# Performance work log

Measured on AMD Instinct MI355X. Metric: run time of the kernel, lower is better.

The kernel has to match this reference:

```python
import jax, jax.numpy as jnp
import numpy as np

NEG_SLOPE = 0.2  # PyG GATConv default leaky_relu slope


def gat_conv(x, src, dst, W, a_src, a_dst, b, num_nodes):
    """One PyG-style GATConv layer (concat over heads).
    x: [N, F_in]; src/dst: [E] (message flows src -> dst);
    W: [F_in, H*C]; a_src/a_dst: [H, C]; b: [H*C].
    """
    H, C = a_src.shape
    h = (x @ W).reshape(num_nodes, H, C)              # [N, H, C]
    alpha_src = jnp.sum(h * a_src, axis=-1)           # [N, H]
    alpha_dst = jnp.sum(h * a_dst, axis=-1)           # [N, H]
    e = jax.nn.leaky_relu(alpha_src[src] + alpha_dst[dst], NEG_SLOPE)  # [E, H]
    # segment softmax over incoming edges of each destination node
    m = jax.ops.segment_max(e, dst, num_segments=num_nodes)            # [N, H]
    ex = jnp.exp(e - m[dst])
    s = jax.ops.segment_sum(ex, dst, num_segments=num_nodes)           # [N, H]
    alpha = ex / (s[dst] + 1e-16)                                      # [E, H]
    msg = h[src] * alpha[:, :, None]                                   # [E, H, C]
    out = jax.ops.segment_sum(msg, dst, num_segments=num_nodes)        # [N, H, C]
    return out.reshape(num_nodes, H * C) + b


def setup_inputs() -> dict:
    key = jax.random.key(0)
    ks = jax.random.split(key, 12)
    N, E, F_in, C, H = 50000, 800000, 256, 64, 8
    x = jax.random.normal(ks[0], (N, F_in), dtype=jnp.float32)
    edge_index = jax.random.randint(ks[1], (2, E), 0, N, dtype=jnp.int64)
    glorot = lambda k, shape: jax.random.normal(k, shape, jnp.float32) * np.sqrt(2.0 / (shape[0] + shape[-1]))
    return {
        "x": x,
        "edge_index": edge_index,
        "W1": glorot(ks[2], (F_in, H * C)),
        "att_src1": glorot(ks[3], (H, C)),
        "att_dst1": glorot(ks[4], (H, C)),
        "b1": jnp.zeros((H * C,), jnp.float32),
        "W2": glorot(ks[5], (H * C, 1 * C)),
        "att_src2": glorot(ks[6], (1, C)),
        "att_dst2": glorot(ks[7], (1, C)),
        "b2": jnp.zeros((C,), jnp.float32),
    }


def reference(x, edge_index, W1, att_src1, att_dst1, b1, W2, att_src2, att_dst2, b2):
    N = x.shape[0]
    # add self-loops (PyG GATConv default add_self_loops=True)
    loops = jnp.arange(N, dtype=edge_index.dtype)
    src = jnp.concatenate([edge_index[0], loops])
    dst = jnp.concatenate([edge_index[1], loops])
    h = gat_conv(x, src, dst, W1, att_src1, att_dst1, b1, N)   # [N, 512]
    h = jax.nn.relu(h)                                         # dropout p=0 -> identity
    out = gat_conv(h, src, dst, W2, att_src2, att_dst2, b2, N) # [N, 64]
    return out
```

## Files before the change

kernel.cpp:

```cpp
#include <hip/hip_runtime.h>
#include <hip/hip_bf16.h>
#include <math.h>
#include <type_traits>

#define NEG_SLOPE 0.2f
#define CAP 64

typedef float f32x4 __attribute__((ext_vector_type(4)));
typedef short s16x8 __attribute__((ext_vector_type(8)));
typedef short s16x4 __attribute__((ext_vector_type(4)));

__device__ __forceinline__ float bf2f(ushort s) {
    union { unsigned u; float f; } cv; cv.u = ((unsigned)s) << 16;
    return cv.f;
}
__device__ __forceinline__ ushort f2bf(float f) {
    __hip_bfloat16 b = __float2bfloat16(f);
    union { __hip_bfloat16 b; ushort u; } cv; cv.b = b;
    return cv.u;
}

__device__ __forceinline__ int edge_val(const int* e, long long i, int is64) {
    return is64 ? e[(size_t)(2 * i)] : e[(size_t)i];
}

__global__ __launch_bounds__(256) void prep_k(
        const float* __restrict__ x, ushort* __restrict__ xb, int NX,
        const float* __restrict__ W1, ushort* __restrict__ W1t, int K1, int N1,
        const float* __restrict__ W2, ushort* __restrict__ W2t, int K2, int N2,
        int nbX, int nbW1) {
    int b = blockIdx.x, tid = threadIdx.x;
    if (b < nbX) {
        int base = (b * 256 + tid) * 8;
        if (base + 8 <= NX) {
            float4 v0 = *(const float4*)&x[base];
            float4 v1 = *(const float4*)&x[base + 4];
            s16x8 w;
            w[0] = (short)f2bf(v0.x); w[1] = (short)f2bf(v0.y);
            w[2] = (short)f2bf(v0.z); w[3] = (short)f2bf(v0.w);
            w[4] = (short)f2bf(v1.x); w[5] = (short)f2bf(v1.y);
            w[6] = (short)f2bf(v1.z); w[7] = (short)f2bf(v1.w);
            *(s16x8*)&xb[base] = w;
        }
        return;
    }
    b -= nbX;
    if (b < nbW1) {
        int idx = b * 256 + tid;
        if (idx < K1 * N1) {
            int k = idx & (K1 - 1), n = idx / K1;
            W1t[(size_t)n * K1 + k] = f2bf(W1[(size_t)k * N1 + n]);
        }
        return;
    }
    b -= nbW1;
    {
        int idx = b * 256 + tid;
        if (idx < K2 * N2) {
            int k = idx & (K2 - 1), n = idx / K2;
            W2t[(size_t)n * K2 + k] = f2bf(W2[(size_t)k * N2 + n]);
        }
    }
}

__global__ __launch_bounds__(256) void scatter_k(
        const int* __restrict__ ebuf, int E, int Nn,
        int* __restrict__ counts, int* __restrict__ csr) {
    __shared__ int s_is64;
    if (threadIdx.x < 64) {
        int v = ebuf[2 * threadIdx.x + 1];
        unsigned long long bl = __ballot(v != 0);
        if (threadIdx.x == 0) s_is64 = (bl == 0ull) ? 1 : 0;
    }
    __syncthreads();
    int is64 = s_is64;
    int i = blockIdx.x * 256 + threadIdx.x;
    if (i >= E + Nn) return;
    int s, d;
    if (i < E) {
        s = edge_val(ebuf, i, is64);
        d = edge_val(ebuf, (long long)E + i, is64);
    } else {
        s = i - E; d = s;
    }
    int pos = atomicAdd(&counts[d], 1);
    if (pos < CAP) csr[(size_t)d * CAP + pos] = s;
}

template <int KK, int NCOLS, int H, int HB>
__global__ __launch_bounds__(512) void gemm_bres(
        const ushort* __restrict__ A, const ushort* __restrict__ Bt,
        ushort* __restrict__ C,
        const float* __restrict__ att_s, const float* __restrict__ att_d,
        float* __restrict__ as_, float* __restrict__ ad_,
        int M, int Ntot) {
    constexpr int NT = NCOLS / 16;
    __shared__ __align__(16) ushort Bs[NCOLS][KK + 8];

    int tid = threadIdx.x;
    int wid = tid >> 6, lane = tid & 63;
    int l15 = lane & 15, l4 = lane >> 4;
    int bx = blockIdx.x, by = blockIdx.y;
    int bn = bx * NCOLS;

#pragma unroll
    for (int p = 0; p < NCOLS * KK / (8 * 512); ++p) {
        int idx = p * 512 + tid;
        int n = idx / (KK / 8);
        int kc = (idx % (KK / 8)) << 3;
        *(s16x8*)&Bs[n][kc] = *(const s16x8*)&Bt[(size_t)(bn + n) * KK + kc];
    }

    int mbase = by * 128 + wid * 16;
    int rowA = mbase + l15; if (rowA >= M) rowA = M - 1;
    const ushort* Ap = A + (size_t)rowA * KK + (l4 << 3);
    s16x8 af[KK / 32];
#pragma unroll
    for (int ks = 0; ks < KK / 32; ++ks) af[ks] = *(const s16x8*)&Ap[ks * 32];

    __syncthreads();

    f32x4 acc[NT] = {};
#pragma unroll
    for (int nt = 0; nt < NT; ++nt) {
#pragma unroll
        for (int ks = 0; ks < KK / 32; ++ks) {
            s16x8 bfr = *(const s16x8*)&Bs[nt * 16 + l15][ks * 32 + (l4 << 3)];
            acc[nt] = __builtin_amdgcn_mfma_f32_16x16x32_bf16(af[ks], bfr, acc[nt], 0, 0, 0);
        }
    }

#pragma unroll
    for (int h = 0; h < HB; ++h) {
        int head = bx * HB + h;
        float asv[4], adv[4];
#pragma unroll
        for (int t = 0; t < 4; ++t) {
            asv[t] = att_s[head * 64 + t * 16 + l15];
            adv[t] = att_d[head * 64 + t * 16 + l15];
        }
#pragma unroll
        for (int j = 0; j < 4; ++j) {
            int r = mbase + (l4 << 2) + j;
            float ps = 0.f, pd = 0.f;
#pragma unroll
            for (int t = 0; t < 4; ++t) {
                float v = acc[h * 4 + t][j];
                ps += v * asv[t];
                pd += v * adv[t];
            }
#pragma unroll
            for (int off = 1; off < 16; off <<= 1) {
                ps += __shfl_xor(ps, off);
                pd += __shfl_xor(pd, off);
            }
            if (r < M) {
                if (l15 == 0) {
                    as_[(size_t)r * H + head] = ps;
                    ad_[(size_t)r * H + head] = pd;
                }
#pragma unroll
                for (int t = 0; t < 4; ++t)
                    C[(size_t)r * Ntot + head * 64 + t * 16 + l15] = f2bf(acc[h * 4 + t][j]);
            }
        }
    }
}

__global__ __launch_bounds__(256) void gat_fused_l1(
        const ushort* __restrict__ h, const float* __restrict__ as_,
        const float* __restrict__ ad_, const int* __restrict__ counts,
        const int* __restrict__ csr, const float* __restrict__ bias,
        ushort* __restrict__ out1, int N) {
    int n = (blockIdx.x * 256 + threadIdx.x) >> 6;
    if (n >= N) return;
    int l = threadIdx.x & 63;
    size_t base = (size_t)n * CAP;
    int deg = counts[n]; deg = deg > CAP ? CAP : deg;

    int hh = l & 7, e0 = l >> 3;
    float adw = ad_[n * 8 + hh];
    float m = -1e30f, s = 0.f;
    for (int k = e0; k < deg; k += 8) {
        int src = csr[base + k];
        float e = as_[src * 8 + hh] + adw;
        e = e > 0.f ? e : NEG_SLOPE * e;
        float mn = fmaxf(m, e);
        s = s * __expf(m - mn) + __expf(e - mn);
        m = mn;
    }
#pragma unroll
    for (int off = 8; off < 64; off <<= 1) {
        float mo = __shfl_xor(m, off), so = __shfl_xor(s, off);
        float mn = fmaxf(m, mo);
        s = s * __expf(m - mn) + so * __expf(mo - mn);
        m = mn;
    }
    float inv = 1.f / (s + 1e-16f);
    int hd = l >> 3;
    float mh   = __shfl(m, hd);
    float invh = __shfl(inv, hd);
    float adh  = __shfl(adw, hd);

    float acc[8] = {};
    int k = 0;
    for (; k + 4 <= deg; k += 4) {
        int s0 = csr[base + k],     s1 = csr[base + k + 1];
        int s2 = csr[base + k + 2], s3 = csr[base + k + 3];
        s16x8 v0 = *(const s16x8*)&h[((size_t)s0 << 9) + (l << 3)];
        s16x8 v1 = *(const s16x8*)&h[((size_t)s1 << 9) + (l << 3)];
        s16x8 v2 = *(const s16x8*)&h[((size_t)s2 << 9) + (l << 3)];
        s16x8 v3 = *(const s16x8*)&h[((size_t)s3 << 9) + (l << 3)];
        float e0v = as_[s0 * 8 + hd] + adh;
        float e1v = as_[s1 * 8 + hd] + adh;
        float e2v = as_[s2 * 8 + hd] + adh;
        float e3v = as_[s3 * 8 + hd] + adh;
        e0v = e0v > 0.f ? e0v : NEG_SLOPE * e0v;
        e1v = e1v > 0.f ? e1v : NEG_SLOPE * e1v;
        e2v = e2v > 0.f ? e2v : NEG_SLOPE * e2v;
        e3v = e3v > 0.f ? e3v : NEG_SLOPE * e3v;
        float a0 = __expf(e0v - mh);
        float a1 = __expf(e1v - mh);
        float a2 = __expf(e2v - mh);
        float a3 = __expf(e3v - mh);
#pragma unroll
        for (int j = 0; j < 8; ++j)
            acc[j] += a0 * bf2f((ushort)v0[j]) + a1 * bf2f((ushort)v1[j])
                    + a2 * bf2f((ushort)v2[j]) + a3 * bf2f((ushort)v3[j]);
    }
    for (; k < deg; ++k) {
        int s0 = csr[base + k];
        s16x8 v0 = *(const s16x8*)&h[((size_t)s0 << 9) + (l << 3)];
        float e0v = as_[s0 * 8 + hd] + adh;
        e0v = e0v > 0.f ? e0v : NEG_SLOPE * e0v;
        float a0 = __expf(e0v - mh);
#pragma unroll
        for (int j = 0; j < 8; ++j) acc[j] += a0 * bf2f((ushort)v0[j]);
    }
    float4 b0 = *(const float4*)&bias[l * 8];
    float4 b1 = *(const float4*)&bias[l * 8 + 4];
    s16x8 w;
    w[0] = f2bf(fmaxf(acc[0] * invh + b0.x, 0.f));
    w[1] = f2bf(fmaxf(acc[1] * invh + b0.y, 0.f));
    w[2] = f2bf(fmaxf(acc[2] * invh + b0.z, 0.f));
    w[3] = f2bf(fmaxf(acc[3] * invh + b0.w, 0.f));
    w[4] = f2bf(fmaxf(acc[4] * invh + b1.x, 0.f));
    w[5] = f2bf(fmaxf(acc[5] * invh + b1.y, 0.f));
    w[6] = f2bf(fmaxf(acc[6] * invh + b1.z, 0.f));
    w[7] = f2bf(fmaxf(acc[7] * invh + b1.w, 0.f));
    *(s16x8*)&out1[((size_t)n << 9) + (l << 3)] = w;
}

__global__ __launch_bounds__(256) void gat_fused_l2(
        const ushort* __restrict__ h, const float* __restrict__ as_,
        const float* __restrict__ ad_, const int* __restrict__ counts,
        const int* __restrict__ csr, const float* __restrict__ bias,
        float* __restrict__ out, int N) {
    int n = (blockIdx.x * 256 + threadIdx.x) >> 6;
    if (n >= N) return;
    int l = threadIdx.x & 63;
    size_t base = (size_t)n * CAP;
    int deg = counts[n]; deg = deg > CAP ? CAP : deg;
    float adv = ad_[n];

    float m = -1e30f, s = 0.f;
    for (int k = l; k < deg; k += 64) {
        float e = as_[csr[base + k]] + adv;
        e = e > 0.f ? e : NEG_SLOPE * e;
        float mn = fmaxf(m, e);
        s = s * __expf(m - mn) + __expf(e - mn);
        m = mn;
    }
#pragma unroll
    for (int off = 1; off < 64; off <<= 1) {
        float mo = __shfl_xor(m, off), so = __shfl_xor(s, off);
        float mn = fmaxf(m, mo);
        s = s * __expf(m - mn) + so * __expf(mo - mn);
        m = mn;
    }
    float inv = 1.f / (s + 1e-16f);

    int q = l >> 4, c4 = l & 15;
    float a0 = 0.f, a1 = 0.f, a2 = 0.f, a3 = 0.f;
    int k = q;
    for (; k + 12 < deg; k += 16) {
        int sA = csr[base + k],     sB = csr[base + k + 4];
        int sC = csr[base + k + 8], sD = csr[base + k + 12];
        s16x4 vA = *(const s16x4*)&h[((size_t)sA << 6) + (c4 << 2)];
        s16x4 vB = *(const s16x4*)&h[((size_t)sB << 6) + (c4 << 2)];
        s16x4 vC = *(const s16x4*)&h[((size_t)sC << 6) + (c4 << 2)];
        s16x4 vD = *(const s16x4*)&h[((size_t)sD << 6) + (c4 << 2)];
        float eA = as_[sA] + adv, eB = as_[sB] + adv;
        float eC = as_[sC] + adv, eD = as_[sD] + adv;
        eA = eA > 0.f ? eA : NEG_SLOPE * eA;
        eB = eB > 0.f ? eB : NEG_SLOPE * eB;
        eC = eC > 0.f ? eC : NEG_SLOPE * eC;
        eD = eD > 0.f ? eD : NEG_SLOPE * eD;
        float aA = __expf(eA - m), aB = __expf(eB - m);
        float aC = __expf(eC - m), aD = __expf(eD - m);
        a0 += aA * bf2f((ushort)vA[0]) + aB * bf2f((ushort)vB[0])
            + aC * bf2f((ushort)vC[0]) + aD * bf2f((ushort)vD[0]);
        a1 += aA * bf2f((ushort)vA[1]) + aB * bf2f((ushort)vB[1])
            + aC * bf2f((ushort)vC[1]) + aD * bf2f((ushort)vD[1]);
        a2 += aA * bf2f((ushort)vA[2]) + aB * bf2f((ushort)vB[2])
            + aC * bf2f((ushort)vC[2]) + aD * bf2f((ushort)vD[2]);
        a3 += aA * bf2f((ushort)vA[3]) + aB * bf2f((ushort)vB[3])
            + aC * bf2f((ushort)vC[3]) + aD * bf2f((ushort)vD[3]);
    }
    for (; k < deg; k += 4) {
        int sA = csr[base + k];
        s16x4 vA = *(const s16x4*)&h[((size_t)sA << 6) + (c4 << 2)];
        float eA = as_[sA] + adv;
        eA = eA > 0.f ? eA : NEG_SLOPE * eA;
        float aA = __expf(eA - m);
        a0 += aA * bf2f((ushort)vA[0]);
        a1 += aA * bf2f((ushort)vA[1]);
        a2 += aA * bf2f((ushort)vA[2]);
        a3 += aA * bf2f((ushort)vA[3]);
    }
    a0 += __shfl_xor(a0, 16); a0 += __shfl_xor(a0, 32);
    a1 += __shfl_xor(a1, 16); a1 += __shfl_xor(a1, 32);
    a2 += __shfl_xor(a2, 16); a2 += __shfl_xor(a2, 32);
    a3 += __shfl_xor(a3, 16); a3 += __shfl_xor(a3, 32);
    if (q == 0) {
        float4 bv = *(const float4*)&bias[c4 << 2];
        float4 r;
        r.x = a0 * inv + bv.x; r.y = a1 * inv + bv.y;
        r.z = a2 * inv + bv.z; r.w = a3 * inv + bv.w;
        *(float4*)&out[((size_t)n << 6) + (c4 << 2)] = r;
    }
}

extern "C" void kernel_launch(void* const* d_in, const int* in_sizes, int n_in,
                              void* d_out, int out_size, void* d_ws, size_t ws_size,
                              hipStream_t stream) {
    const float* x    = (const float*)d_in[0];
    const int*   ebuf = (const int*)d_in[1];
    const float* W1   = (const float*)d_in[2];
    const float* aS1  = (const float*)d_in[3];
    const float* aD1  = (const float*)d_in[4];
    const float* b1   = (const float*)d_in[5];
    const float* W2   = (const float*)d_in[6];
    const float* aS2  = (const float*)d_in[7];
    const float* aD2  = (const float*)d_in[8];
    const float* b2   = (const float*)d_in[9];
    float* out = (float*)d_out;

    const int F_in = 256, H1 = 8, HC1 = 512, C2 = 64;
    int N = in_sizes[0] / F_in;
    int E = in_sizes[1] / 2;
    int NX = N * F_in;

    char* ws = (char*)d_ws;
    size_t off = 0;
    auto alloc = [&](size_t bytes) -> void* {
        void* p = ws + off;
        off = (off + bytes + 255) & ~(size_t)255;
        return p;
    };
    ushort* h1b    = (ushort*)alloc((size_t)N * HC1 * 2);
    ushort* out1b  = (ushort*)alloc((size_t)N * HC1 * 2);
    float* as1     = (float*)alloc((size_t)N * H1 * 4);
    float* ad1     = (float*)alloc((size_t)N * H1 * 4);
    float* as2     = (float*)alloc((size_t)N * 4);
    float* ad2     = (float*)alloc((size_t)N * 4);
    int*   counts  = (int*)alloc((size_t)N * 4);
    int*   csr     = (int*)alloc((size_t)N * CAP * 4);
    ushort* W1t    = (ushort*)alloc((size_t)F_in * HC1 * 2);
    ushort* W2t    = (ushort*)alloc((size_t)HC1 * C2 * 2);
    ushort* h2b    = h1b;
    ushort* xb     = out1b;

    int nbX  = (NX + 2047) / 2048;
    int nbW1 = (F_in * HC1 + 255) >> 8;
    int nbW2 = (HC1 * C2 + 255) >> 8;
    int nbScat = (E + N + 255) / 256;

    hipMemsetAsync(counts, 0, (size_t)N * 4, stream);

    prep_k<<<nbX + nbW1 + nbW2, 256, 0, stream>>>(
        x, xb, NX, W1, W1t, F_in, HC1, W2, W2t, HC1, C2, nbX, nbW1);

    scatter_k<<<nbScat, 256, 0, stream>>>(ebuf, E, N, counts, csr);

    {
        dim3 g(2, (N + 127) / 128);
        gemm_bres<256, 256, 8, 4><<<g, 512, 0, stream>>>(
            xb, W1t, h1b, aS1, aD1, as1, ad1, N, HC1);
    }

    gat_fused_l1<<<(N + 3) / 4, 256, 0, stream>>>(h1b, as1, ad1, counts, csr, b1, out1b, N);

    {
        dim3 g(1, (N + 127) / 128);
        gemm_bres<512, 64, 1, 1><<<g, 512, 0, stream>>>(
            out1b, W2t, h2b, aS2, aD2, as2, ad2, N, C2);
    }

    gat_fused_l2<<<(N + 3) / 4, 256, 0, stream>>>(h2b, as2, ad2, counts, csr, b2, out, N);
}
```

Baseline: 306.6 us.

## Fuse x bf16 conversion into GEMM1 and co-launch edge scatter with it

The separate x-to-bf16 conversion pass is removed: GEMM1 now reads fp32 x directly and converts it in registers. The CSR scatter kernel is merged into the same launch as GEMM1, so scatter blocks can run alongside GEMM blocks, and the counts memset moves into the weight-prep kernel. GEMM block indices are remapped so the two column tiles sharing a row block are scheduled near each other for A reuse. In exchange, GEMM1 reads twice as many bytes of A, and a shared-memory allocation may now be reserved for scatter blocks too.

After: 288.0 us. -6.1%, faster.

```diff
diff --git a/kernel.cpp b/kernel.cpp
--- a/kernel.cpp
+++ b/kernel.cpp
@@ -25,26 +25,10 @@
 }
 
 __global__ __launch_bounds__(256) void prep_k(
-        const float* __restrict__ x, ushort* __restrict__ xb, int NX,
         const float* __restrict__ W1, ushort* __restrict__ W1t, int K1, int N1,
         const float* __restrict__ W2, ushort* __restrict__ W2t, int K2, int N2,
-        int nbX, int nbW1) {
+        int* __restrict__ counts, int N, int nbW1, int nbW2) {
     int b = blockIdx.x, tid = threadIdx.x;
-    if (b < nbX) {
-        int base = (b * 256 + tid) * 8;
-        if (base + 8 <= NX) {
-            float4 v0 = *(const float4*)&x[base];
-            float4 v1 = *(const float4*)&x[base + 4];
-            s16x8 w;
-            w[0] = (short)f2bf(v0.x); w[1] = (short)f2bf(v0.y);
-            w[2] = (short)f2bf(v0.z); w[3] = (short)f2bf(v0.w);
-            w[4] = (short)f2bf(v1.x); w[5] = (short)f2bf(v1.y);
-            w[6] = (short)f2bf(v1.z); w[7] = (short)f2bf(v1.w);
-            *(s16x8*)&xb[base] = w;
-        }
-        return;
-    }
-    b -= nbX;
     if (b < nbW1) {
         int idx = b * 256 + tid;
         if (idx < K1 * N1) {
@@ -54,53 +38,31 @@
         return;
     }
     b -= nbW1;
-    {
+    if (b < nbW2) {
         int idx = b * 256 + tid;
         if (idx < K2 * N2) {
             int k = idx & (K2 - 1), n = idx / K2;
             W2t[(size_t)n * K2 + k] = f2bf(W2[(size_t)k * N2 + n]);
         }
-    }
-}
-
-__global__ __launch_bounds__(256) void scatter_k(
-        const int* __restrict__ ebuf, int E, int Nn,
-        int* __restrict__ counts, int* __restrict__ csr) {
-    __shared__ int s_is64;
-    if (threadIdx.x < 64) {
-        int v = ebuf[2 * threadIdx.x + 1];
-        unsigned long long bl = __ballot(v != 0);
-        if (threadIdx.x == 0) s_is64 = (bl == 0ull) ? 1 : 0;
-    }
-    __syncthreads();
-    int is64 = s_is64;
-    int i = blockIdx.x * 256 + threadIdx.x;
-    if (i >= E + Nn) return;
-    int s, d;
-    if (i < E) {
-        s = edge_val(ebuf, i, is64);
-        d = edge_val(ebuf, (long long)E + i, is64);
-    } else {
-        s = i - E; d = s;
-    }
-    int pos = atomicAdd(&counts[d], 1);
-    if (pos < CAP) csr[(size_t)d * CAP + pos] = s;
-}
-
-template <int KK, int NCOLS, int H, int HB>
-__global__ __launch_bounds__(512) void gemm_bres(
-        const ushort* __restrict__ A, const ushort* __restrict__ Bt,
+        return;
+    }
+    b -= nbW2;
+    int i = b * 256 + tid;
+    if (i < N) counts[i] = 0;
+}
+
+template <typename AT, int KK, int NCOLS, int H, int HB>
+__device__ __forceinline__ void gemm_bres_core(
+        int bx, int by, const AT* __restrict__ A, const ushort* __restrict__ Bt,
         ushort* __restrict__ C,
         const float* __restrict__ att_s, const float* __restrict__ att_d,
-        float* __restrict__ as_, float* __restrict__ ad_,
-        int M, int Ntot) {
+        float* __restrict__ as_, float* __restrict__ ad_, int M, int Ntot) {
     constexpr int NT = NCOLS / 16;
     __shared__ __align__(16) ushort Bs[NCOLS][KK + 8];
 
     int tid = threadIdx.x;
     int wid = tid >> 6, lane = tid & 63;
     int l15 = lane & 15, l4 = lane >> 4;
-    int bx = blockIdx.x, by = blockIdx.y;
     int bn = bx * NCOLS;
 
 #pragma unroll
@@ -113,10 +75,25 @@
 
     int mbase = by * 128 + wid * 16;
     int rowA = mbase + l15; if (rowA >= M) rowA = M - 1;
-    const ushort* Ap = A + (size_t)rowA * KK + (l4 << 3);
     s16x8 af[KK / 32];
-#pragma unroll
-    for (int ks = 0; ks < KK / 32; ++ks) af[ks] = *(const s16x8*)&Ap[ks * 32];
+    if constexpr (std::is_same_v<AT, float>) {
+        const float* Ap = A + (size_t)rowA * KK + (l4 << 3);
+#pragma unroll
+        for (int ks = 0; ks < KK / 32; ++ks) {
+            float4 u0 = *(const float4*)&Ap[ks * 32];
+            float4 u1 = *(const float4*)&Ap[ks * 32 + 4];
+            s16x8 w;
+            w[0] = (short)f2bf(u0.x); w[1] = (short)f2bf(u0.y);
+            w[2] = (short)f2bf(u0.z); w[3] = (short)f2bf(u0.w);
+            w[4] = (short)f2bf(u1.x); w[5] = (short)f2bf(u1.y);
+            w[6] = (short)f2bf(u1.z); w[7] = (short)f2bf(u1.w);
+            af[ks] = w;
+        }
+    } else {
+        const ushort* Ap = A + (size_t)rowA * KK + (l4 << 3);
+#pragma unroll
+        for (int ks = 0; ks < KK / 32; ++ks) af[ks] = *(const s16x8*)&Ap[ks * 32];
+    }
 
     __syncthreads();
 
@@ -165,6 +142,52 @@
             }
         }
     }
+}
+
+__global__ __launch_bounds__(512) void gemm1_scatter(
+        const float* __restrict__ A, const ushort* __restrict__ Bt,
+        ushort* __restrict__ C, const float* __restrict__ att_s,
+        const float* __restrict__ att_d, float* __restrict__ as_,
+        float* __restrict__ ad_, int M, int Ntot, int nby, int nGemm,
+        const int* __restrict__ ebuf, int E, int Nn,
+        int* __restrict__ counts, int* __restrict__ csr) {
+    int g = blockIdx.x;
+    if (g < nGemm) {
+        int by = (g & 7) + ((g >> 4) << 3);
+        int bx = (g >> 3) & 1;
+        if (by < nby)
+            gemm_bres_core<float, 256, 256, 8, 4>(bx, by, A, Bt, C,
+                                                  att_s, att_d, as_, ad_, M, Ntot);
+        return;
+    }
+    __shared__ int s_is64;
+    if (threadIdx.x < 64) {
+        int v = ebuf[2 * threadIdx.x + 1];
+        unsigned long long bl = __ballot(v != 0);
+        if (threadIdx.x == 0) s_is64 = (bl == 0ull) ? 1 : 0;
+    }
+    __syncthreads();
+    int is64 = s_is64;
+    int i = (g - nGemm) * 512 + threadIdx.x;
+    if (i >= E + Nn) return;
+    int s, d;
+    if (i < E) {
+        s = edge_val(ebuf, i, is64);
+        d = edge_val(ebuf, (long long)E + i, is64);
+    } else {
+        s = i - E; d = s;
+    }
+    int pos = atomicAdd(&counts[d], 1);
+    if (pos < CAP) csr[(size_t)d * CAP + pos] = s;
+}
+
+template <typename AT, int KK, int NCOLS, int H, int HB>
+__global__ __launch_bounds__(512) void gemm_bres(
+        const AT* __restrict__ A, const ushort* __restrict__ Bt, ushort* __restrict__ C,
+        const float* __restrict__ att_s, const float* __restrict__ att_d,
+        float* __restrict__ as_, float* __restrict__ ad_, int M, int Ntot) {
+    gemm_bres_core<AT, KK, NCOLS, H, HB>(blockIdx.x, blockIdx.y, A, Bt, C,
+                                         att_s, att_d, as_, ad_, M, Ntot);
 }
 
 __global__ __launch_bounds__(256) void gat_fused_l1(
@@ -349,7 +372,6 @@
     const int F_in = 256, H1 = 8, HC1 = 512, C2 = 64;
     int N = in_sizes[0] / F_in;
     int E = in_sizes[1] / 2;
-    int NX = N * F_in;
 
     char* ws = (char*)d_ws;
     size_t off = 0;
@@ -369,31 +391,29 @@
     ushort* W1t    = (ushort*)alloc((size_t)F_in * HC1 * 2);
     ushort* W2t    = (ushort*)alloc((size_t)HC1 * C2 * 2);
     ushort* h2b    = h1b;
-    ushort* xb     = out1b;
-
-    int nbX  = (NX + 2047) / 2048;
+
     int nbW1 = (F_in * HC1 + 255) >> 8;
     int nbW2 = (HC1 * C2 + 255) >> 8;
-    int nbScat = (E + N + 255) / 256;
-
-    hipMemsetAsync(counts, 0, (size_t)N * 4, stream);
-
-    prep_k<<<nbX + nbW1 + nbW2, 256, 0, stream>>>(
-        x, xb, NX, W1, W1t, F_in, HC1, W2, W2t, HC1, C2, nbX, nbW1);
-
-    scatter_k<<<nbScat, 256, 0, stream>>>(ebuf, E, N, counts, csr);
+    int nbZ  = (N + 255) >> 8;
+
+    prep_k<<<nbW1 + nbW2 + nbZ, 256, 0, stream>>>(
+        W1, W1t, F_in, HC1, W2, W2t, HC1, C2, counts, N, nbW1, nbW2);
 
     {
-        dim3 g(2, (N + 127) / 128);
-        gemm_bres<256, 256, 8, 4><<<g, 512, 0, stream>>>(
-            xb, W1t, h1b, aS1, aD1, as1, ad1, N, HC1);
+        int nby = (N + 127) / 128;
+        int nbyPad = (nby + 7) & ~7;
+        int nGemm = 2 * nbyPad;
+        int nScatter = (E + N + 511) / 512;
+        gemm1_scatter<<<nGemm + nScatter, 512, 0, stream>>>(
+            x, W1t, h1b, aS1, aD1, as1, ad1, N, HC1, nby, nGemm,
+            ebuf, E, N, counts, csr);
     }
 
     gat_fused_l1<<<(N + 3) / 4, 256, 0, stream>>>(h1b, as1, ad1, counts, csr, b1, out1b, N);
 
     {
         dim3 g(1, (N + 127) / 128);
-        gemm_bres<512, 64, 1, 1><<<g, 512, 0, stream>>>(
+        gemm_bres<ushort, 512, 64, 1, 1><<<g, 512, 0, stream>>>(
             out1b, W2t, h2b, aS2, aD2, as2, ad2, N, C2);
     }
 
```
